# Optimization experiments

Hardware: AMD Instinct MI355X
Metric: run time of the kernel (lower is better)

## Reference

```python
import jax, jax.numpy as jnp
import numpy as np

N_E = 8192
E_DIM = 256
BETA = 0.25


def setup_inputs() -> dict:
    key = jax.random.key(0)
    k1, k2 = jax.random.split(key)
    z = jax.random.normal(k1, (8, E_DIM, 32, 32), dtype=jnp.float32)
    # nn.Embedding default init: N(0, 1)
    W = jax.random.normal(k2, (N_E, E_DIM), dtype=jnp.float32)
    return {"z": z, "W": W}


def reference(z, W):
    # logits: (B, n_e, H, W)
    logits = jnp.einsum('bdhw,nd->bnhw', z, W)
    soft_one_hot = jax.nn.softmax(logits, axis=1)
    ind = jnp.argmax(soft_one_hot, axis=1)  # (B, H, W)
    hard_one_hot = jax.nn.one_hot(ind, N_E, axis=1, dtype=logits.dtype)  # (B, n_e, H, W)
    # straight-through estimator
    one_hot = hard_one_hot - jax.lax.stop_gradient(soft_one_hot) + soft_one_hot
    z_q = jnp.einsum('bnhw,nd->bdhw', one_hot, W)
    z_q_2 = jnp.einsum('bnhw,nd->bdhw', hard_one_hot, W)
    quant_loss = (jnp.mean((z_q - z) ** 2)
                  + jnp.mean((jax.lax.stop_gradient(z_q_2) - z) ** 2)
                  + BETA * jnp.mean((z_q_2 - jax.lax.stop_gradient(z)) ** 2))
    ind_flat = jnp.reshape(ind, (-1,))
    return z_q, quant_loss, ind_flat
```

## Files before the change

### kernel.cpp

```cpp
#include <hip/hip_runtime.h>
#include <math.h>


using short8  = __attribute__((ext_vector_type(8))) short;
using floatx4 = __attribute__((ext_vector_type(4))) float;

#define MARGIN 0.5f
#define APAD   264

__device__ inline unsigned short f2bf(float x) {
    union { float f; unsigned u; } v; v.f = x;
    unsigned r = v.u + 0x7fffu + ((v.u >> 16) & 1u);
    return (unsigned short)(r >> 16);
}
__device__ inline unsigned f2ord(float f) {
    unsigned u = __float_as_uint(f);
    return (u & 0x80000000u) ? ~u : (u | 0x80000000u);
}
__device__ inline float ord2f(unsigned o) {
    return __uint_as_float((o & 0x80000000u) ? (o ^ 0x80000000u) : ~o);
}

__global__ void convert_kernel(const float* __restrict__ W, const float* __restrict__ z,
                               unsigned short* __restrict__ wb, unsigned short* __restrict__ zb) {
    if (blockIdx.x < 2048) {
        int i = blockIdx.x * 256 + threadIdx.x;
        float4 v = *(const float4*)&W[(size_t)i * 4];
        ushort4 o;
        o.x = f2bf(v.x); o.y = f2bf(v.y); o.z = f2bf(v.z); o.w = f2bf(v.w);
        *(ushort4*)&wb[(size_t)i * 4] = o;
    } else {
        __shared__ float tile[64 * 65];
        int blk = blockIdx.x - 2048;
        int b  = blk >> 6;
        int dt = (blk >> 4) & 3;
        int st = blk & 15;
        int dl = threadIdx.x >> 6, sl = threadIdx.x & 63;
#pragma unroll
        for (int i = 0; i < 16; ++i) {
            int d = i * 4 + dl;
            tile[sl * 65 + d] = z[(size_t)b * 262144 + (size_t)(dt * 64 + d) * 1024 + st * 64 + sl];
        }
        __syncthreads();
        int d2 = threadIdx.x & 63, sr = threadIdx.x >> 6;
#pragma unroll
        for (int i = 0; i < 16; ++i) {
            int s = i * 4 + sr;
            int pos = b * 1024 + st * 64 + s;
            zb[(size_t)pos * 256 + dt * 64 + d2] = f2bf(tile[s * 65 + d2]);
        }
    }
}

__global__ __launch_bounds__(512, 2)
void gemm_argmax_kernel(const unsigned short* __restrict__ zb,
                        const unsigned short* __restrict__ wb,
                        uint2* __restrict__ part)
{
    __shared__ unsigned short As[128 * APAD];
    __shared__ unsigned short Bs[2][256 * 32];

    const int t  = threadIdx.x;
    const int bm = blockIdx.x, bn = blockIdx.y;
    const int w  = t >> 6, lane = t & 63;
    const int wm = w >> 2, wn = w & 3;
    const int q  = lane >> 4, l15 = lane & 15;

    const unsigned short* wsrc = wb + (size_t)bn * 2048 * 256;

#pragma unroll
    for (int i = 0; i < 2; ++i) {
        int u = i * 512 + t;
        int code = u >> 2, q2 = u & 3;
        int ksw = (q2 ^ ((code >> 1) & 3)) * 8;
        const unsigned short* g = wsrc + (size_t)code * 256 + ksw;
        __builtin_amdgcn_global_load_lds(
            (const __attribute__((address_space(1))) void*)g,
            (__attribute__((address_space(3))) void*)(&Bs[0][u * 8]),
            16, 0, 0);
    }

    {
        const unsigned short* src = zb + (size_t)bm * 128 * 256;
#pragma unroll
        for (int i = 0; i < 8; ++i) {
            int u = i * 512 + t;
            int row = u >> 5, c8 = (u & 31) * 8;
            *(short8*)(&As[row * APAD + c8]) = *(const short8*)(src + row * 256 + c8);
        }
    }
    __syncthreads();

    unsigned kkey[4][4];
    floatx4  acc[4][4];
#pragma unroll
    for (int im = 0; im < 4; ++im)
#pragma unroll
        for (int r = 0; r < 4; ++r) {
            kkey[im][r] = 0u;
            floatx4 zz = {0.f, 0.f, 0.f, 0.f};
            acc[im][r] = zz;
        }

#pragma unroll 2
    for (int pc = 0; pc < 64; ++pc) {
        const int cur = pc & 1, kp = pc & 7;

        if (pc < 63) {
            const int np = pc + 1, nnc = np >> 3, nkp = np & 7, nxt = np & 1;
#pragma unroll
            for (int i = 0; i < 2; ++i) {
                int u = i * 512 + t;
                int code = u >> 2, q2 = u & 3;
                int ksw = (q2 ^ ((code >> 1) & 3)) * 8;
                const unsigned short* g =
                    wsrc + (size_t)(nnc * 256 + code) * 256 + nkp * 32 + ksw;
                __builtin_amdgcn_global_load_lds(
                    (const __attribute__((address_space(1))) void*)g,
                    (__attribute__((address_space(3))) void*)(&Bs[nxt][u * 8]),
                    16, 0, 0);
            }
        }

        short8 af[4], bfr[4];
#pragma unroll
        for (int im = 0; im < 4; ++im)
            af[im] = *(const short8*)&As[(wm * 64 + im * 16 + l15) * APAD + kp * 32 + q * 8];
#pragma unroll
        for (int in = 0; in < 4; ++in) {
            int row = wn * 64 + in * 16 + l15;
            bfr[in] = *(const short8*)&Bs[cur][row * 32 + (q ^ ((row >> 1) & 3)) * 8];
        }
#pragma unroll
        for (int im = 0; im < 4; ++im)
#pragma unroll
            for (int in = 0; in < 4; ++in)
                acc[im][in] = __builtin_amdgcn_mfma_f32_16x16x32_bf16(
                    af[im], bfr[in], acc[im][in], 0, 0, 0);

        if ((pc & 7) == 7) {
            const int nc = pc >> 3;
            const int nbase = bn * 2048 + nc * 256 + wn * 64 + l15;
#pragma unroll
            for (int im = 0; im < 4; ++im)
#pragma unroll
                for (int r = 0; r < 4; ++r) {
                    float bv = acc[im][0][r];
                    int   bi = nbase;
#pragma unroll
                    for (int in = 1; in < 4; ++in) {
                        float v = acc[im][in][r];
                        int   n = nbase + in * 16;
                        bi = (v > bv) ? n : bi;
                        bv = (v > bv) ? v : bv;
                    }
                    unsigned key = (f2ord(bv) & 0xFFFFE000u) | (8191u - (unsigned)bi);
                    kkey[im][r] = (key > kkey[im][r]) ? key : kkey[im][r];
#pragma unroll
                    for (int in = 0; in < 4; ++in) acc[im][in][r] = 0.f;
                }
        }
        __syncthreads();
    }

#pragma unroll
    for (int im = 0; im < 4; ++im)
#pragma unroll
        for (int r = 0; r < 4; ++r) {
            unsigned k1 = kkey[im][r], k2 = 0u;
#pragma unroll
            for (int off = 1; off < 16; off <<= 1) {
                unsigned o1 = (unsigned)__shfl_xor((int)k1, off, 64);
                unsigned o2 = (unsigned)__shfl_xor((int)k2, off, 64);
                unsigned hi = (k1 > o1) ? k1 : o1;
                unsigned lo = (k1 > o1) ? o1 : k1;
                unsigned s2 = (k2 > o2) ? k2 : o2;
                k1 = hi;
                k2 = (lo > s2) ? lo : s2;
            }
            if (l15 == 0) {
                int pos = bm * 128 + wm * 64 + im * 16 + q * 4 + r;
                part[(size_t)pos * 16 + bn * 4 + wn] = make_uint2(k1, k2);
            }
        }
}

__global__ __launch_bounds__(256, 4)
void resolve_kernel(const float* __restrict__ z, const float* __restrict__ W,
                    const uint2* __restrict__ part,
                    float* __restrict__ zq, float* __restrict__ loss,
                    float* __restrict__ ind)
{
    __shared__ float wq[16 * 260];
    __shared__ int   best[16];
    __shared__ float lred[4];

    const int t = threadIdx.x, w = t >> 6, lane = t & 63;
    const int pos0 = blockIdx.x * 16;
    const int b = pos0 >> 10, s0 = pos0 & 1023;

#pragma unroll
    for (int i = 0; i < 4; ++i) {
        const int pl = w * 4 + i;
        const int p  = pos0 + pl;
        uint2 rec = part[(size_t)p * 16 + (lane & 15)];
        unsigned k1 = rec.x, k2 = rec.y;

        unsigned kmax = (k1 > k2) ? k1 : k2;
#pragma unroll
        for (int off = 1; off < 64; off <<= 1) {
            unsigned o = (unsigned)__shfl_xor((int)kmax, off, 64);
            kmax = (o > kmax) ? o : kmax;
        }
        const float vmax = ord2f(kmax & 0xFFFFE000u);
        const float thr  = vmax - MARGIN;

        int cl = 0;
        if (lane < 16) {
            float h1 = ord2f((k1 & 0xFFFFE000u) + 0x2000u);
            float h2 = ord2f((k2 & 0xFFFFE000u) + 0x2000u);
            cl = ((h1 >= thr) ? 1 : 0) + ((h2 >= thr) ? 1 : 0);
        }
#pragma unroll
        for (int off = 1; off < 64; off <<= 1) cl += __shfl_xor(cl, off, 64);

        int bi;
        if (cl <= 1) {
            bi = 8191 - (int)(kmax & 8191u);
        } else {
            const float* zp = z + (size_t)b * 262144 + (p & 1023);
            float zf0 = zp[(size_t)(lane * 4 + 0) * 1024];
            float zf1 = zp[(size_t)(lane * 4 + 1) * 1024];
            float zf2 = zp[(size_t)(lane * 4 + 2) * 1024];
            float zf3 = zp[(size_t)(lane * 4 + 3) * 1024];
            float bv = -INFINITY; bi = 0x7FFFFFFF;
            for (int s16 = 0; s16 < 16; ++s16) {
                unsigned kk[2];
                kk[0] = (unsigned)__shfl((int)k1, s16, 64);
                kk[1] = (unsigned)__shfl((int)k2, s16, 64);
#pragma unroll
                for (int h = 0; h < 2; ++h) {
                    float vh = ord2f((kk[h] & 0xFFFFE000u) + 0x2000u);
                    if (vh < thr) continue;
                    int c = 8191 - (int)(kk[h] & 8191u);
                    float4 wf = *(const float4*)&W[(size_t)c * 256 + lane * 4];
                    float d = zf0 * wf.x + zf1 * wf.y + zf2 * wf.z + zf3 * wf.w;
#pragma unroll
                    for (int off = 1; off < 64; off <<= 1) d += __shfl_xor(d, off, 64);
                    if (d > bv || (d == bv && c < bi)) { bv = d; bi = c; }
                }
            }
        }
        if (lane == 0) { best[pl] = bi; ind[p] = (float)bi; }
    }
    __syncthreads();

    {
        int r = t >> 4, c = t & 15;
#pragma unroll
        for (int j = 0; j < 4; ++j) {
            int d = c * 4 + j * 64;
            *(float4*)&wq[r * 260 + d] = *(const float4*)&W[(size_t)best[r] * 256 + d];
        }
    }
    __syncthreads();

    {
        int sl = t & 15, dg = t >> 4;
        float ls = 0.f;
#pragma unroll
        for (int it = 0; it < 4; ++it) {
            int d = it * 64 + dg * 4;
            float4 wv = *(const float4*)&wq[sl * 260 + d];
            const float* zp = z  + (size_t)b * 262144 + (size_t)d * 1024 + s0 + sl;
            float*       qp = zq + (size_t)b * 262144 + (size_t)d * 1024 + s0 + sl;
            float z0 = zp[0], z1 = zp[1024], z2 = zp[2048], z3 = zp[3072];
            qp[0] = wv.x; qp[1024] = wv.y; qp[2048] = wv.z; qp[3072] = wv.w;
            float d0 = wv.x - z0, d1 = wv.y - z1, d2 = wv.z - z2, d3 = wv.w - z3;
            ls += d0 * d0 + d1 * d1 + d2 * d2 + d3 * d3;
        }
#pragma unroll
        for (int off = 1; off < 64; off <<= 1) ls += __shfl_xor(ls, off, 64);
        if (lane == 0) lred[w] = ls;
    }
    __syncthreads();
    if (t == 0)
        atomicAdd(loss, (lred[0] + lred[1] + lred[2] + lred[3]) * (2.25f / 2097152.0f));
}

#define TP 16
#define ZPAD 260
#define WPAD 36
__global__ __launch_bounds__(256, 2)
void vq_kernel(const float* __restrict__ z, const float* __restrict__ W,
               float* __restrict__ zq, float* __restrict__ loss,
               float* __restrict__ ind)
{
    __shared__ float zs[TP * ZPAD];
    __shared__ float ws[256 * WPAD];
    __shared__ int   best[TP];
    __shared__ float lred[4];
    const int t = threadIdx.x, w = t >> 6, lane = t & 63, cg = t & 63;
    const int pos_base = blockIdx.x * TP;
    const int b = pos_base >> 10, s0 = pos_base & 1023;
    const float* zb = z + (size_t)b * 262144 + s0;
    { int p = t & 15, dg = t >> 4;
      for (int i = 0; i < 16; ++i) { int d = i * 16 + dg; zs[p * ZPAD + d] = zb[(size_t)d * 1024 + p]; } }
    float maxv[4]; int maxi[4];
#pragma unroll
    for (int i = 0; i < 4; ++i) { maxv[i] = -INFINITY; maxi[i] = 0; }
    for (int cc = 0; cc < 32; ++cc) {
        float acc[4][4];
#pragma unroll
        for (int i = 0; i < 4; ++i)
#pragma unroll
            for (int j = 0; j < 4; ++j) acc[i][j] = 0.0f;
        for (int kp = 0; kp < 8; ++kp) {
            __syncthreads();
#pragma unroll
            for (int i = 0; i < 8; ++i) {
                int f = i * 256 + t, code = f >> 3, k4 = f & 7;
                float4 v = *(const float4*)&W[(size_t)(cc * 256 + code) * 256 + kp * 32 + k4 * 4];
                *(float4*)&ws[code * WPAD + k4 * 4] = v;
            }
            __syncthreads();
#pragma unroll
            for (int k4 = 0; k4 < 8; ++k4) {
                float4 zf[4], wf[4];
#pragma unroll
                for (int i = 0; i < 4; ++i) zf[i] = *(const float4*)&zs[(w * 4 + i) * ZPAD + kp * 32 + k4 * 4];
#pragma unroll
                for (int j = 0; j < 4; ++j) wf[j] = *(const float4*)&ws[(cg + 64 * j) * WPAD + k4 * 4];
#pragma unroll
                for (int i = 0; i < 4; ++i)
#pragma unroll
                    for (int j = 0; j < 4; ++j) {
                        acc[i][j] += zf[i].x * wf[j].x; acc[i][j] += zf[i].y * wf[j].y;
                        acc[i][j] += zf[i].z * wf[j].z; acc[i][j] += zf[i].w * wf[j].w;
                    }
            }
        }
#pragma unroll
        for (int i = 0; i < 4; ++i)
#pragma unroll
            for (int j = 0; j < 4; ++j) {
                int code = cc * 256 + cg + 64 * j; float v = acc[i][j];
                if (v > maxv[i] || (v == maxv[i] && code < maxi[i])) { maxv[i] = v; maxi[i] = code; }
            }
    }
#pragma unroll
    for (int i = 0; i < 4; ++i) {
        float v = maxv[i]; int idx = maxi[i];
        for (int off = 32; off > 0; off >>= 1) {
            float ov = __shfl_down(v, off, 64); int oi = __shfl_down(idx, off, 64);
            if (ov > v || (ov == v && oi < idx)) { v = ov; idx = oi; }
        }
        if (lane == 0) { int p = w * 4 + i; best[p] = idx; ind[pos_base + p] = (float)idx; }
    }
    __syncthreads();
    float lsum = 0.0f;
    for (int p = 0; p < TP; ++p) {
        int bi = best[p];
        float wv = W[(size_t)bi * 256 + t];
        float zv = zs[p * ZPAD + t];
        float dd = wv - zv; lsum += dd * dd;
        zq[(size_t)b * 262144 + (size_t)t * 1024 + s0 + p] = wv;
    }
    for (int off = 32; off > 0; off >>= 1) lsum += __shfl_down(lsum, off, 64);
    if (lane == 0) lred[w] = lsum;
    __syncthreads();
    if (t == 0) atomicAdd(loss, (lred[0] + lred[1] + lred[2] + lred[3]) * (2.25f / 2097152.0f));
}

extern "C" void kernel_launch(void* const* d_in, const int* in_sizes, int n_in,
                              void* d_out, int out_size, void* d_ws, size_t ws_size,
                              hipStream_t stream) {
    const float* z = (const float*)d_in[0];
    const float* W = (const float*)d_in[1];
    float* out  = (float*)d_out;
    float* zq   = out;
    float* loss = out + 2097152;
    float* ind  = out + 2097153;

    hipMemsetAsync(loss, 0, sizeof(float), stream);

    if (ws_size >= (size_t)10 * 1024 * 1024) {
        unsigned short* zbuf = (unsigned short*)d_ws;
        unsigned short* wbuf = zbuf + 2097152;
        uint2* part = (uint2*)((char*)d_ws + (size_t)8 * 1024 * 1024);
        convert_kernel<<<2560, 256, 0, stream>>>(W, z, wbuf, zbuf);
        gemm_argmax_kernel<<<dim3(64, 4), 512, 0, stream>>>(zbuf, wbuf, part);
        resolve_kernel<<<512, 256, 0, stream>>>(z, W, part, zq, loss, ind);
    } else {
        vq_kernel<<<512, 256, 0, stream>>>(z, W, zq, loss, ind);
    }
}
```

Measured before the change: 141.1 us.

## Load codebook fragments directly into registers and drop per-step LDS staging

The GEMM kernel no longer stages W tiles through shared memory with async global-to-LDS loads and a barrier every k-step. Each wave now loads its own B fragments straight from global memory into a two-deep register double buffer, prefetching two steps ahead, and the loop is fully unrolled with no __syncthreads. The loss zeroing moves from a separate memset into the convert kernel, which removes one launch. The trade-off is more register pressure and uncoalesced per-lane global loads that rely on L2 hits, since four wm-rows of waves each load the same B fragments.

```diff
diff --git a/kernel.cpp b/kernel.cpp
--- a/kernel.cpp
+++ b/kernel.cpp
@@ -22,8 +22,10 @@
 }
 
 __global__ void convert_kernel(const float* __restrict__ W, const float* __restrict__ z,
-                               unsigned short* __restrict__ wb, unsigned short* __restrict__ zb) {
+                               unsigned short* __restrict__ wb, unsigned short* __restrict__ zb,
+                               float* __restrict__ loss) {
     if (blockIdx.x < 2048) {
+        if (blockIdx.x == 0 && threadIdx.x == 0) *loss = 0.f;
         int i = blockIdx.x * 256 + threadIdx.x;
         float4 v = *(const float4*)&W[(size_t)i * 4];
         ushort4 o;
@@ -58,7 +60,6 @@
                         uint2* __restrict__ part)
 {
     __shared__ unsigned short As[128 * APAD];
-    __shared__ unsigned short Bs[2][256 * 32];
 
     const int t  = threadIdx.x;
     const int bm = blockIdx.x, bn = blockIdx.y;
@@ -66,19 +67,16 @@
     const int wm = w >> 2, wn = w & 3;
     const int q  = lane >> 4, l15 = lane & 15;
 
-    const unsigned short* wsrc = wb + (size_t)bn * 2048 * 256;
-
-#pragma unroll
-    for (int i = 0; i < 2; ++i) {
-        int u = i * 512 + t;
-        int code = u >> 2, q2 = u & 3;
-        int ksw = (q2 ^ ((code >> 1) & 3)) * 8;
-        const unsigned short* g = wsrc + (size_t)code * 256 + ksw;
-        __builtin_amdgcn_global_load_lds(
-            (const __attribute__((address_space(1))) void*)g,
-            (__attribute__((address_space(3))) void*)(&Bs[0][u * 8]),
-            16, 0, 0);
-    }
+    const unsigned short* bwave =
+        wb + (size_t)(bn * 2048 + wn * 64 + l15) * 256 + q * 8;
+
+    short8 bf[2][4];
+#pragma unroll
+    for (int in = 0; in < 4; ++in)
+        bf[0][in] = *(const short8*)(bwave + (size_t)in * 16 * 256);
+#pragma unroll
+    for (int in = 0; in < 4; ++in)
+        bf[1][in] = *(const short8*)(bwave + (size_t)in * 16 * 256 + 32);
 
     {
         const unsigned short* src = zb + (size_t)bm * 128 * 256;
@@ -102,41 +100,28 @@
             acc[im][r] = zz;
         }
 
-#pragma unroll 2
+#pragma unroll
     for (int pc = 0; pc < 64; ++pc) {
         const int cur = pc & 1, kp = pc & 7;
 
-        if (pc < 63) {
-            const int np = pc + 1, nnc = np >> 3, nkp = np & 7, nxt = np & 1;
-#pragma unroll
-            for (int i = 0; i < 2; ++i) {
-                int u = i * 512 + t;
-                int code = u >> 2, q2 = u & 3;
-                int ksw = (q2 ^ ((code >> 1) & 3)) * 8;
-                const unsigned short* g =
-                    wsrc + (size_t)(nnc * 256 + code) * 256 + nkp * 32 + ksw;
-                __builtin_amdgcn_global_load_lds(
-                    (const __attribute__((address_space(1))) void*)g,
-                    (__attribute__((address_space(3))) void*)(&Bs[nxt][u * 8]),
-                    16, 0, 0);
-            }
-        }
-
-        short8 af[4], bfr[4];
+        short8 af[4];
 #pragma unroll
         for (int im = 0; im < 4; ++im)
             af[im] = *(const short8*)&As[(wm * 64 + im * 16 + l15) * APAD + kp * 32 + q * 8];
 #pragma unroll
-        for (int in = 0; in < 4; ++in) {
-            int row = wn * 64 + in * 16 + l15;
-            bfr[in] = *(const short8*)&Bs[cur][row * 32 + (q ^ ((row >> 1) & 3)) * 8];
-        }
-#pragma unroll
         for (int im = 0; im < 4; ++im)
 #pragma unroll
             for (int in = 0; in < 4; ++in)
                 acc[im][in] = __builtin_amdgcn_mfma_f32_16x16x32_bf16(
-                    af[im], bfr[in], acc[im][in], 0, 0, 0);
+                    af[im], bf[cur][in], acc[im][in], 0, 0, 0);
+
+        if (pc + 2 < 64) {
+            const int np = pc + 2, nnc = np >> 3, nkp = np & 7;
+            const size_t off = (size_t)nnc * 256 * 256 + nkp * 32;
+#pragma unroll
+            for (int in = 0; in < 4; ++in)
+                bf[cur][in] = *(const short8*)(bwave + off + (size_t)in * 16 * 256);
+        }
 
         if ((pc & 7) == 7) {
             const int nc = pc >> 3;
@@ -160,7 +145,6 @@
                     for (int in = 0; in < 4; ++in) acc[im][in][r] = 0.f;
                 }
         }
-        __syncthreads();
     }
 
 #pragma unroll
@@ -382,16 +366,15 @@
     float* loss = out + 2097152;
     float* ind  = out + 2097153;
 
-    hipMemsetAsync(loss, 0, sizeof(float), stream);
-
     if (ws_size >= (size_t)10 * 1024 * 1024) {
         unsigned short* zbuf = (unsigned short*)d_ws;
         unsigned short* wbuf = zbuf + 2097152;
         uint2* part = (uint2*)((char*)d_ws + (size_t)8 * 1024 * 1024);
-        convert_kernel<<<2560, 256, 0, stream>>>(W, z, wbuf, zbuf);
+        convert_kernel<<<2560, 256, 0, stream>>>(W, z, wbuf, zbuf, loss);
         gemm_argmax_kernel<<<dim3(64, 4), 512, 0, stream>>>(zbuf, wbuf, part);
         resolve_kernel<<<512, 256, 0, stream>>>(z, W, part, zq, loss, ind);
     } else {
+        hipMemsetAsync(loss, 0, sizeof(float), stream);
         vq_kernel<<<512, 256, 0, stream>>>(z, W, zq, loss, ind);
     }
 }
```

New measurement: 253.5 us. +79.7%, slower.
